# Optimization experiments

Hardware: AMD Instinct MI355X
Metric: run time of the kernel (lower is better)

## Reference

```python
import jax, jax.numpy as jnp
import numpy as np

INPUT_DIM = 256
EMBED_DIM = 256
NUM_HEADS = 8
HEAD_DIM = EMBED_DIM // NUM_HEADS
N_TOKENS = 11136
N_BATCH = 16


def _xavier(key, shape):
    fan_out, fan_in = shape
    bound = np.sqrt(6.0 / (fan_in + fan_out)).astype(np.float32)
    return jax.random.uniform(key, shape, jnp.float32, -bound, bound)


def setup_inputs() -> dict:
    key = jax.random.key(0)
    k_x, k_ids, k_qkv, k_o = jax.random.split(key, 4)
    x = jax.random.normal(k_x, (N_TOKENS, INPUT_DIM), jnp.float32)
    batch_ids = jnp.sort(jax.random.randint(k_ids, (N_TOKENS,), 0, N_BATCH)).astype(jnp.int32)
    qkv_w = _xavier(k_qkv, (3 * EMBED_DIM, INPUT_DIM))
    qkv_b = jnp.zeros((3 * EMBED_DIM,), jnp.float32)
    o_w = _xavier(k_o, (EMBED_DIM, EMBED_DIM))
    o_b = jnp.zeros((EMBED_DIM,), jnp.float32)
    return {"x": x, "batch_ids": batch_ids, "qkv_w": qkv_w, "qkv_b": qkv_b,
            "o_w": o_w, "o_b": o_b}


def reference(x, batch_ids, qkv_w, qkv_b, o_w, o_b):
    # batch_ids is concrete metadata (mirrors np.unique on CPU in the original).
    ids = np.asarray(batch_ids)
    vals, counts = np.unique(ids, return_counts=True)
    B = len(vals)
    S = int(counts.max())
    offsets = np.concatenate([np.zeros(1, np.int64), np.cumsum(counts)[:-1]])
    seg = np.searchsorted(vals, ids)               # segment index per token
    pos = np.arange(ids.shape[0]) - offsets[seg]   # position within segment

    qkv = x @ qkv_w.T + qkv_b                      # [N, 3E]
    # pad_sequence with padding_value=1 -> scatter tokens into an all-ones buffer
    fin = jnp.ones((B, S, 3 * EMBED_DIM), qkv.dtype).at[seg, pos].set(qkv)
    # padded rows sum to exactly 3E (all ones) -> mask True marks padding
    pad_mask = fin.sum(-1) >= fin.shape[-1]        # [B, S]

    qkv4 = fin.reshape(B, S, NUM_HEADS, 3 * HEAD_DIM).transpose(0, 2, 1, 3)
    q, k, v = jnp.split(qkv4, 3, axis=-1)          # each [B, H, S, hd]

    logits = jnp.einsum('bhqd,bhkd->bhqk', q, k) * (HEAD_DIM ** -0.5)
    logits = jnp.where(pad_mask[:, None, None, :], -jnp.inf, logits)
    attn = jax.nn.softmax(logits, axis=-1)         # [B, H, S, S]

    out = jnp.einsum('bhqk,bhkd->bhqd', attn, v)
    out = out.transpose(0, 2, 1, 3).reshape(B, S, EMBED_DIM)
    out = out[seg, pos]                            # unpad -> [N, E]
    return out @ o_w.T + o_b
```

## Files before the change

### kernel.cpp

```cpp
#include <hip/hip_runtime.h>
#include <stdint.h>


#define N_TOK 11136
#define E 256
#define H 8
#define HD 32

typedef __attribute__((ext_vector_type(8))) __bf16 bf16x8;
typedef __attribute__((ext_vector_type(8))) unsigned short u16x8;
typedef __attribute__((ext_vector_type(4))) float f32x4;

__device__ __forceinline__ unsigned short f2bf(float f) {
  unsigned int u = __float_as_uint(f);
  u = (u + 0x7FFFu + ((u >> 16) & 1u)) >> 16;
  return (unsigned short)u;
}
__device__ __forceinline__ float bf2f(unsigned short s) {
  return __uint_as_float(((unsigned int)s) << 16);
}
__device__ __forceinline__ bf16x8 ld8(const unsigned short* p) {
  return *(const bf16x8*)p;
}

__global__ void k_offsets(const int* __restrict__ ids, int* __restrict__ offs) {
  int b = threadIdx.x;
  if (b > 16) return;
  int lo = 0, hi = N_TOK;
  while (lo < hi) { int mid = (lo + hi) >> 1; if (ids[mid] < b) lo = mid + 1; else hi = mid; }
  offs[b] = lo;
}

#define QK_BSTRIDE 264
#define QSCALE (0.17677669529663687f * 1.4426950408889634f)
__global__ __launch_bounds__(256, 3) void k_qkv(
    const float* __restrict__ x, const float* __restrict__ qw,
    const float* __restrict__ qkv_b,
    unsigned short* __restrict__ Qb, unsigned short* __restrict__ Kb,
    unsigned short* __restrict__ Vt) {
  __shared__ __align__(16) unsigned short Bhi[48 * QK_BSTRIDE];
  __shared__ __align__(16) unsigned short Blo[48 * QK_BSTRIDE];
  int tid = threadIdx.x;
  int w = tid >> 6, lane = tid & 63, m = lane & 15, quad = lane >> 4;
  int col0 = blockIdx.y * 48;

  {
    const float4* qw4 = (const float4*)(qw + (size_t)col0 * E);
#pragma unroll
    for (int i = 0; i < 12; ++i) {
      int flat = i * 256 + tid;
      float4 v = qw4[flat];
      int row = flat >> 6, kq = flat & 63;
      ushort4 hv, lv;
      hv.x = f2bf(v.x); lv.x = f2bf(v.x - bf2f(hv.x));
      hv.y = f2bf(v.y); lv.y = f2bf(v.y - bf2f(hv.y));
      hv.z = f2bf(v.z); lv.z = f2bf(v.z - bf2f(hv.z));
      hv.w = f2bf(v.w); lv.w = f2bf(v.w - bf2f(hv.w));
      *(ushort4*)(Bhi + row * QK_BSTRIDE + kq * 4) = hv;
      *(ushort4*)(Blo + row * QK_BSTRIDE + kq * 4) = lv;
    }
  }
  __syncthreads();

  int base = blockIdx.x * 64 + w * 16;
  const float* ap = x + (size_t)(base + m) * E;
  f32x4 acc[3] = {};
  float4 c0 = *(const float4*)(ap + quad * 8);
  float4 c1 = *(const float4*)(ap + quad * 8 + 4);
  for (int kc = 0; kc < 8; ++kc) {
    float4 u0 = c0, u1 = c1;
    if (kc < 7) {
      c0 = *(const float4*)(ap + (kc + 1) * 32 + quad * 8);
      c1 = *(const float4*)(ap + (kc + 1) * 32 + quad * 8 + 4);
    }
    int ko = kc * 32 + quad * 8;
    float vv[8] = {u0.x, u0.y, u0.z, u0.w, u1.x, u1.y, u1.z, u1.w};
    u16x8 hr, lr_;
#pragma unroll
    for (int i = 0; i < 8; ++i) {
      unsigned short hh = f2bf(vv[i]);
      hr[i] = hh;
      lr_[i] = f2bf(vv[i] - bf2f(hh));
    }
    bf16x8 ah = __builtin_bit_cast(bf16x8, hr);
    bf16x8 al = __builtin_bit_cast(bf16x8, lr_);
#pragma unroll
    for (int t = 0; t < 3; ++t) {
      bf16x8 bh = ld8(Bhi + (16 * t + m) * QK_BSTRIDE + ko);
      bf16x8 bl = ld8(Blo + (16 * t + m) * QK_BSTRIDE + ko);
      acc[t] = __builtin_amdgcn_mfma_f32_16x16x32_bf16(ah, bh, acc[t], 0, 0, 0);
      acc[t] = __builtin_amdgcn_mfma_f32_16x16x32_bf16(ah, bl, acc[t], 0, 0, 0);
      acc[t] = __builtin_amdgcn_mfma_f32_16x16x32_bf16(al, bh, acc[t], 0, 0, 0);
    }
  }
#pragma unroll
  for (int t = 0; t < 3; ++t) {
    int j = col0 + 16 * t + m;
    int hd = j / 96;
    int rr = j - hd * 96;
    float bias = qkv_b[j];
    int tokb = base + quad * 4;
    if (rr < 64) {
      float qsc = (rr < 32) ? QSCALE : 1.0f;
      unsigned short* dst = (rr < 32) ? (Qb + (size_t)hd * N_TOK * HD + rr)
                                      : (Kb + (size_t)hd * N_TOK * HD + (rr - 32));
#pragma unroll
      for (int r = 0; r < 4; ++r)
        dst[(size_t)(tokb + r) * HD] = f2bf((acc[t][r] + bias) * qsc);
    } else {
      int d = rr - 64;
      ushort4 pk;
      pk.x = f2bf(acc[t][0] + bias); pk.y = f2bf(acc[t][1] + bias);
      pk.z = f2bf(acc[t][2] + bias); pk.w = f2bf(acc[t][3] + bias);
      *(ushort4*)(Vt + (size_t)(hd * HD + d) * N_TOK + tokb) = pk;
    }
  }
}

#define PSTRIDE 72
__global__ __launch_bounds__(256, 4) void k_attn(
    const int* __restrict__ ids, const int* __restrict__ offs,
    const unsigned short* __restrict__ Qb, const unsigned short* __restrict__ Kb,
    const unsigned short* __restrict__ Vt,
    unsigned short* __restrict__ attnb) {
  __shared__ __align__(16) unsigned short Kl[2][64 * 32];
  __shared__ __align__(16) unsigned short Vl[2][32 * 64];
  __shared__ __align__(16) unsigned short ldsP[4][16 * PSTRIDE];
  __shared__ int bred[8];
  int tid = threadIdx.x;
  int w = tid >> 6, lane = tid & 63;
  int m = lane & 15, quad = lane >> 4;
  int h = blockIdx.y;
  int tok0 = blockIdx.x * 64;
  int q0 = tok0 + w * 16;
  unsigned short* P = ldsP[w];
  int tok = q0 + m;
  int b = ids[tok];
  int st = offs[b], en = offs[b + 1];
  int kmin = st, kmax = en, stM = st, enm = en;
#pragma unroll
  for (int d = 1; d <= 8; d <<= 1) {
    kmin = min(kmin, __shfl_xor(kmin, d));
    kmax = max(kmax, __shfl_xor(kmax, d));
    stM  = max(stM,  __shfl_xor(stM,  d));
    enm  = min(enm,  __shfl_xor(enm,  d));
  }
  if (lane == 0) { bred[w] = kmin; bred[4 + w] = kmax; }
  __syncthreads();
  int kminB = min(min(bred[0], bred[1]), min(bred[2], bred[3]));
  int kmaxB = max(max(bred[4], bred[5]), max(bred[6], bred[7]));
  int k0beg = kminB & ~63;

  const unsigned short* Kbase = Qb ? Kb + (size_t)h * N_TOK * HD : Kb;
  const unsigned short* Vbase = Vt + (size_t)h * HD * N_TOK;
  bf16x8 qf = ld8(Qb + (size_t)(h * N_TOK + tok) * HD + quad * 8);

  int krow = w * 16 + (lane >> 2);
  int kgof = (lane & 3) * 8;
  int vrow = w * 8 + (lane >> 3);
  int vgof = (lane & 7) * 8;

  bf16x8 kg = ld8(Kbase + (size_t)(k0beg + krow) * HD + kgof);
  bf16x8 vg = ld8(Vbase + (size_t)vrow * N_TOK + k0beg + vgof);
  *(bf16x8*)(&Kl[0][krow * 32 + kgof]) = kg;
  *(bf16x8*)(&Vl[0][vrow * 64 + vgof]) = vg;
  __syncthreads();

  float lsum = 0.f;
  f32x4 o0 = {}, o1 = {};
  int buf = 0;
  for (int k0 = k0beg; k0 < kmaxB; k0 += 64) {
    int k1 = (k0 + 64 < kmaxB) ? (k0 + 64) : k0;
    kg = ld8(Kbase + (size_t)(k1 + krow) * HD + kgof);
    vg = ld8(Vbase + (size_t)vrow * N_TOK + k1 + vgof);
    const unsigned short* Kc = &Kl[buf][0];
    const unsigned short* Vc = &Vl[buf][0];
    f32x4 s[4];
#pragma unroll
    for (int i = 0; i < 4; ++i) {
      bf16x8 kf = ld8(Kc + (16 * i + m) * 32 + quad * 8);
      f32x4 z = {};
      s[i] = __builtin_amdgcn_mfma_f32_16x16x32_bf16(kf, qf, z, 0, 0, 0);
    }
    bool interior = (k0 >= stM && k0 + 64 <= enm);
    int jb = k0 + quad * 4;
#pragma unroll
    for (int i = 0; i < 4; ++i) {
      float p[4];
#pragma unroll
      for (int r = 0; r < 4; ++r) {
        float sv = s[i][r];
        if (!interior) {
          int j = jb + 16 * i + r;
          sv = (j >= st && j < en) ? sv : -3e38f;
        }
        float e;
        asm("v_exp_f32 %0, %1" : "=v"(e) : "v"(sv));
        p[r] = e;
      }
      lsum += (p[0] + p[1]) + (p[2] + p[3]);
      unsigned int b0 = __float_as_uint(p[0]) + 0x8000u;
      unsigned int b1 = __float_as_uint(p[1]) + 0x8000u;
      unsigned int b2 = __float_as_uint(p[2]) + 0x8000u;
      unsigned int b3 = __float_as_uint(p[3]) + 0x8000u;
      uint2 pk;
      pk.x = (b1 & 0xFFFF0000u) | (b0 >> 16);
      pk.y = (b3 & 0xFFFF0000u) | (b2 >> 16);
      *(uint2*)(P + m * PSTRIDE + 16 * i + quad * 4) = pk;
    }
#pragma unroll
    for (int c = 0; c < 2; ++c) {
      bf16x8 pf  = ld8(P + m * PSTRIDE + 32 * c + quad * 8);
      bf16x8 vf0 = ld8(Vc + m * 64 + 32 * c + quad * 8);
      bf16x8 vf1 = ld8(Vc + (16 + m) * 64 + 32 * c + quad * 8);
      o0 = __builtin_amdgcn_mfma_f32_16x16x32_bf16(vf0, pf, o0, 0, 0, 0);
      o1 = __builtin_amdgcn_mfma_f32_16x16x32_bf16(vf1, pf, o1, 0, 0, 0);
    }
    *(bf16x8*)(&Kl[buf ^ 1][krow * 32 + kgof]) = kg;
    *(bf16x8*)(&Vl[buf ^ 1][vrow * 64 + vgof]) = vg;
    __syncthreads();
    buf ^= 1;
  }
  lsum += __shfl_xor(lsum, 16);
  lsum += __shfl_xor(lsum, 32);
  float inv = 1.0f / lsum;
  ushort4 pk0, pk1;
  pk0.x = f2bf(o0[0] * inv); pk0.y = f2bf(o0[1] * inv);
  pk0.z = f2bf(o0[2] * inv); pk0.w = f2bf(o0[3] * inv);
  pk1.x = f2bf(o1[0] * inv); pk1.y = f2bf(o1[1] * inv);
  pk1.z = f2bf(o1[2] * inv); pk1.w = f2bf(o1[3] * inv);
  *(ushort4*)(attnb + (size_t)tok * E + h * HD + quad * 4) = pk0;
  *(ushort4*)(attnb + (size_t)tok * E + h * HD + 16 + quad * 4) = pk1;
}

__global__ __launch_bounds__(256, 2) void k_oproj(
    const unsigned short* __restrict__ attnb, const float* __restrict__ ow,
    const float* __restrict__ ob, float* __restrict__ out) {
  __shared__ __align__(16) unsigned short Bo[64 * QK_BSTRIDE];
  int tid = threadIdx.x;
  int w = tid >> 6, lane = tid & 63, m = lane & 15, quad = lane >> 4;
  int tok0 = blockIdx.x * 64, col0 = blockIdx.y * 64;
  {
    const float4* ow4 = (const float4*)(ow + (size_t)col0 * E);
#pragma unroll
    for (int i = 0; i < 16; ++i) {
      int flat = i * 256 + tid;
      float4 v = ow4[flat];
      int row = flat >> 6, kq = flat & 63;
      ushort4 hv;
      hv.x = f2bf(v.x); hv.y = f2bf(v.y); hv.z = f2bf(v.z); hv.w = f2bf(v.w);
      *(ushort4*)(Bo + row * QK_BSTRIDE + kq * 4) = hv;
    }
  }
  __syncthreads();
  f32x4 acc[4] = {};
  int arow = tok0 + 16 * w + m;
  for (int kc = 0; kc < 8; ++kc) {
    int ko = kc * 32 + quad * 8;
    bf16x8 a = ld8(attnb + (size_t)arow * E + ko);
#pragma unroll
    for (int t = 0; t < 4; ++t) {
      bf16x8 b = ld8(Bo + (16 * t + m) * QK_BSTRIDE + ko);
      acc[t] = __builtin_amdgcn_mfma_f32_16x16x32_bf16(a, b, acc[t], 0, 0, 0);
    }
  }
#pragma unroll
  for (int t = 0; t < 4; ++t) {
    int j = col0 + 16 * t + m;
    float bias = ob[j];
#pragma unroll
    for (int r = 0; r < 4; ++r) {
      int tok = tok0 + 16 * w + quad * 4 + r;
      out[(size_t)tok * E + j] = acc[t][r] + bias;
    }
  }
}

extern "C" void kernel_launch(void* const* d_in, const int* in_sizes, int n_in,
                              void* d_out, int out_size, void* d_ws, size_t ws_size,
                              hipStream_t stream) {
  const float* x   = (const float*)d_in[0];
  const int*   ids = (const int*)d_in[1];
  const float* qw  = (const float*)d_in[2];
  const float* qb  = (const float*)d_in[3];
  const float* ow  = (const float*)d_in[4];
  const float* ob  = (const float*)d_in[5];
  float* out = (float*)d_out;

  char* p = (char*)d_ws;
  auto alloc = [&](size_t bytes) {
    char* r = p;
    p += (bytes + 255) & ~(size_t)255;
    return r;
  };
  int* offs = (int*)alloc(32 * sizeof(int));
  unsigned short* Qb  = (unsigned short*)alloc((size_t)N_TOK * E * 2);
  unsigned short* Kb  = (unsigned short*)alloc((size_t)N_TOK * E * 2);
  unsigned short* Vt  = (unsigned short*)alloc((size_t)N_TOK * E * 2);
  unsigned short* att = (unsigned short*)alloc((size_t)N_TOK * E * 2);

  k_offsets<<<dim3(1), dim3(64), 0, stream>>>(ids, offs);
  k_qkv<<<dim3(N_TOK / 64, 16), dim3(256), 0, stream>>>(x, qw, qb, Qb, Kb, Vt);
  k_attn<<<dim3(N_TOK / 64, H), dim3(256), 0, stream>>>(ids, offs, Qb, Kb, Vt, att);
  k_oproj<<<dim3(N_TOK / 64, E / 64), dim3(256), 0, stream>>>(att, ow, ob, out);
}
```

Before: 163.2 us.

## Pre-split inputs and weights to bf16 hi/lo in a separate kernel

```diff
diff --git a/kernel.cpp b/kernel.cpp
--- a/kernel.cpp
+++ b/kernel.cpp
@@ -31,10 +31,49 @@
   offs[b] = lo;
 }
 
+__global__ void k_split(const float* __restrict__ x, const float* __restrict__ qw,
+                        const float* __restrict__ ow,
+                        unsigned short* __restrict__ xhi, unsigned short* __restrict__ xlo,
+                        unsigned short* __restrict__ whi, unsigned short* __restrict__ wlo,
+                        unsigned short* __restrict__ owb) {
+  const int NX4 = N_TOK * E / 4;
+  const int NW4 = 3 * E * E / 4;
+  const int NO4 = E * E / 4;
+  int total = NX4 + NW4 + NO4;
+  for (int i = blockIdx.x * blockDim.x + threadIdx.x; i < total;
+       i += gridDim.x * blockDim.x) {
+    if (i < NX4) {
+      float4 v = ((const float4*)x)[i];
+      ushort4 hv, lv;
+      hv.x = f2bf(v.x); lv.x = f2bf(v.x - bf2f(hv.x));
+      hv.y = f2bf(v.y); lv.y = f2bf(v.y - bf2f(hv.y));
+      hv.z = f2bf(v.z); lv.z = f2bf(v.z - bf2f(hv.z));
+      hv.w = f2bf(v.w); lv.w = f2bf(v.w - bf2f(hv.w));
+      ((ushort4*)xhi)[i] = hv; ((ushort4*)xlo)[i] = lv;
+    } else if (i < NX4 + NW4) {
+      int j = i - NX4;
+      float4 v = ((const float4*)qw)[j];
+      ushort4 hv, lv;
+      hv.x = f2bf(v.x); lv.x = f2bf(v.x - bf2f(hv.x));
+      hv.y = f2bf(v.y); lv.y = f2bf(v.y - bf2f(hv.y));
+      hv.z = f2bf(v.z); lv.z = f2bf(v.z - bf2f(hv.z));
+      hv.w = f2bf(v.w); lv.w = f2bf(v.w - bf2f(hv.w));
+      ((ushort4*)whi)[j] = hv; ((ushort4*)wlo)[j] = lv;
+    } else {
+      int j = i - NX4 - NW4;
+      float4 v = ((const float4*)ow)[j];
+      ushort4 hv;
+      hv.x = f2bf(v.x); hv.y = f2bf(v.y); hv.z = f2bf(v.z); hv.w = f2bf(v.w);
+      ((ushort4*)owb)[j] = hv;
+    }
+  }
+}
+
 #define QK_BSTRIDE 264
 #define QSCALE (0.17677669529663687f * 1.4426950408889634f)
 __global__ __launch_bounds__(256, 3) void k_qkv(
-    const float* __restrict__ x, const float* __restrict__ qw,
+    const unsigned short* __restrict__ xhi, const unsigned short* __restrict__ xlo,
+    const unsigned short* __restrict__ whi, const unsigned short* __restrict__ wlo,
     const float* __restrict__ qkv_b,
     unsigned short* __restrict__ Qb, unsigned short* __restrict__ Kb,
     unsigned short* __restrict__ Vt) {
@@ -42,55 +81,42 @@
   __shared__ __align__(16) unsigned short Blo[48 * QK_BSTRIDE];
   int tid = threadIdx.x;
   int w = tid >> 6, lane = tid & 63, m = lane & 15, quad = lane >> 4;
-  int col0 = blockIdx.y * 48;
+  int col0 = blockIdx.x * 48;
+  int base0 = blockIdx.y * 128;
 
   {
-    const float4* qw4 = (const float4*)(qw + (size_t)col0 * E);
-#pragma unroll
-    for (int i = 0; i < 12; ++i) {
+    const u16x8* wh8 = (const u16x8*)(whi + (size_t)col0 * E);
+    const u16x8* wl8 = (const u16x8*)(wlo + (size_t)col0 * E);
+#pragma unroll
+    for (int i = 0; i < 6; ++i) {
       int flat = i * 256 + tid;
-      float4 v = qw4[flat];
-      int row = flat >> 6, kq = flat & 63;
-      ushort4 hv, lv;
-      hv.x = f2bf(v.x); lv.x = f2bf(v.x - bf2f(hv.x));
-      hv.y = f2bf(v.y); lv.y = f2bf(v.y - bf2f(hv.y));
-      hv.z = f2bf(v.z); lv.z = f2bf(v.z - bf2f(hv.z));
-      hv.w = f2bf(v.w); lv.w = f2bf(v.w - bf2f(hv.w));
-      *(ushort4*)(Bhi + row * QK_BSTRIDE + kq * 4) = hv;
-      *(ushort4*)(Blo + row * QK_BSTRIDE + kq * 4) = lv;
+      int row = flat >> 5, c8 = flat & 31;
+      *(u16x8*)(Bhi + row * QK_BSTRIDE + c8 * 8) = wh8[flat];
+      *(u16x8*)(Blo + row * QK_BSTRIDE + c8 * 8) = wl8[flat];
     }
   }
   __syncthreads();
 
-  int base = blockIdx.x * 64 + w * 16;
-  const float* ap = x + (size_t)(base + m) * E;
-  f32x4 acc[3] = {};
-  float4 c0 = *(const float4*)(ap + quad * 8);
-  float4 c1 = *(const float4*)(ap + quad * 8 + 4);
+  f32x4 acc[2][3] = {};
   for (int kc = 0; kc < 8; ++kc) {
-    float4 u0 = c0, u1 = c1;
-    if (kc < 7) {
-      c0 = *(const float4*)(ap + (kc + 1) * 32 + quad * 8);
-      c1 = *(const float4*)(ap + (kc + 1) * 32 + quad * 8 + 4);
-    }
     int ko = kc * 32 + quad * 8;
-    float vv[8] = {u0.x, u0.y, u0.z, u0.w, u1.x, u1.y, u1.z, u1.w};
-    u16x8 hr, lr_;
-#pragma unroll
-    for (int i = 0; i < 8; ++i) {
-      unsigned short hh = f2bf(vv[i]);
-      hr[i] = hh;
-      lr_[i] = f2bf(vv[i] - bf2f(hh));
-    }
-    bf16x8 ah = __builtin_bit_cast(bf16x8, hr);
-    bf16x8 al = __builtin_bit_cast(bf16x8, lr_);
+    bf16x8 ah[2], al[2];
+#pragma unroll
+    for (int mt = 0; mt < 2; ++mt) {
+      int arow = base0 + mt * 64 + w * 16 + m;
+      ah[mt] = ld8(xhi + (size_t)arow * E + ko);
+      al[mt] = ld8(xlo + (size_t)arow * E + ko);
+    }
 #pragma unroll
     for (int t = 0; t < 3; ++t) {
       bf16x8 bh = ld8(Bhi + (16 * t + m) * QK_BSTRIDE + ko);
       bf16x8 bl = ld8(Blo + (16 * t + m) * QK_BSTRIDE + ko);
-      acc[t] = __builtin_amdgcn_mfma_f32_16x16x32_bf16(ah, bh, acc[t], 0, 0, 0);
-      acc[t] = __builtin_amdgcn_mfma_f32_16x16x32_bf16(ah, bl, acc[t], 0, 0, 0);
-      acc[t] = __builtin_amdgcn_mfma_f32_16x16x32_bf16(al, bh, acc[t], 0, 0, 0);
+#pragma unroll
+      for (int mt = 0; mt < 2; ++mt) {
+        acc[mt][t] = __builtin_amdgcn_mfma_f32_16x16x32_bf16(ah[mt], bh, acc[mt][t], 0, 0, 0);
+        acc[mt][t] = __builtin_amdgcn_mfma_f32_16x16x32_bf16(ah[mt], bl, acc[mt][t], 0, 0, 0);
+        acc[mt][t] = __builtin_amdgcn_mfma_f32_16x16x32_bf16(al[mt], bh, acc[mt][t], 0, 0, 0);
+      }
     }
   }
 #pragma unroll
@@ -99,20 +125,23 @@
     int hd = j / 96;
     int rr = j - hd * 96;
     float bias = qkv_b[j];
-    int tokb = base + quad * 4;
-    if (rr < 64) {
-      float qsc = (rr < 32) ? QSCALE : 1.0f;
-      unsigned short* dst = (rr < 32) ? (Qb + (size_t)hd * N_TOK * HD + rr)
-                                      : (Kb + (size_t)hd * N_TOK * HD + (rr - 32));
-#pragma unroll
-      for (int r = 0; r < 4; ++r)
-        dst[(size_t)(tokb + r) * HD] = f2bf((acc[t][r] + bias) * qsc);
-    } else {
-      int d = rr - 64;
-      ushort4 pk;
-      pk.x = f2bf(acc[t][0] + bias); pk.y = f2bf(acc[t][1] + bias);
-      pk.z = f2bf(acc[t][2] + bias); pk.w = f2bf(acc[t][3] + bias);
-      *(ushort4*)(Vt + (size_t)(hd * HD + d) * N_TOK + tokb) = pk;
+#pragma unroll
+    for (int mt = 0; mt < 2; ++mt) {
+      int tokb = base0 + mt * 64 + w * 16 + quad * 4;
+      if (rr < 64) {
+        float qsc = (rr < 32) ? QSCALE : 1.0f;
+        unsigned short* dst = (rr < 32) ? (Qb + (size_t)hd * N_TOK * HD + rr)
+                                        : (Kb + (size_t)hd * N_TOK * HD + (rr - 32));
+#pragma unroll
+        for (int r = 0; r < 4; ++r)
+          dst[(size_t)(tokb + r) * HD] = f2bf((acc[mt][t][r] + bias) * qsc);
+      } else {
+        int d = rr - 64;
+        ushort4 pk;
+        pk.x = f2bf(acc[mt][t][0] + bias); pk.y = f2bf(acc[mt][t][1] + bias);
+        pk.z = f2bf(acc[mt][t][2] + bias); pk.w = f2bf(acc[mt][t][3] + bias);
+        *(ushort4*)(Vt + (size_t)(hd * HD + d) * N_TOK + tokb) = pk;
+      }
     }
   }
 }
@@ -151,7 +180,7 @@
   int kmaxB = max(max(bred[4], bred[5]), max(bred[6], bred[7]));
   int k0beg = kminB & ~63;
 
-  const unsigned short* Kbase = Qb ? Kb + (size_t)h * N_TOK * HD : Kb;
+  const unsigned short* Kbase = Kb + (size_t)h * N_TOK * HD;
   const unsigned short* Vbase = Vt + (size_t)h * HD * N_TOK;
   bf16x8 qf = ld8(Qb + (size_t)(h * N_TOK + tok) * HD + quad * 8);
 
@@ -234,22 +263,19 @@
 }
 
 __global__ __launch_bounds__(256, 2) void k_oproj(
-    const unsigned short* __restrict__ attnb, const float* __restrict__ ow,
+    const unsigned short* __restrict__ attnb, const unsigned short* __restrict__ owb,
     const float* __restrict__ ob, float* __restrict__ out) {
   __shared__ __align__(16) unsigned short Bo[64 * QK_BSTRIDE];
   int tid = threadIdx.x;
   int w = tid >> 6, lane = tid & 63, m = lane & 15, quad = lane >> 4;
   int tok0 = blockIdx.x * 64, col0 = blockIdx.y * 64;
   {
-    const float4* ow4 = (const float4*)(ow + (size_t)col0 * E);
-#pragma unroll
-    for (int i = 0; i < 16; ++i) {
+    const u16x8* o8 = (const u16x8*)(owb + (size_t)col0 * E);
+#pragma unroll
+    for (int i = 0; i < 8; ++i) {
       int flat = i * 256 + tid;
-      float4 v = ow4[flat];
-      int row = flat >> 6, kq = flat & 63;
-      ushort4 hv;
-      hv.x = f2bf(v.x); hv.y = f2bf(v.y); hv.z = f2bf(v.z); hv.w = f2bf(v.w);
-      *(ushort4*)(Bo + row * QK_BSTRIDE + kq * 4) = hv;
+      int row = flat >> 5, c8 = flat & 31;
+      *(u16x8*)(Bo + row * QK_BSTRIDE + c8 * 8) = o8[flat];
     }
   }
   __syncthreads();
@@ -294,13 +320,19 @@
     return r;
   };
   int* offs = (int*)alloc(32 * sizeof(int));
+  unsigned short* xhi = (unsigned short*)alloc((size_t)N_TOK * E * 2);
+  unsigned short* xlo = (unsigned short*)alloc((size_t)N_TOK * E * 2);
+  unsigned short* whi = (unsigned short*)alloc((size_t)3 * E * E * 2);
+  unsigned short* wlo = (unsigned short*)alloc((size_t)3 * E * E * 2);
+  unsigned short* owb = (unsigned short*)alloc((size_t)E * E * 2);
   unsigned short* Qb  = (unsigned short*)alloc((size_t)N_TOK * E * 2);
   unsigned short* Kb  = (unsigned short*)alloc((size_t)N_TOK * E * 2);
   unsigned short* Vt  = (unsigned short*)alloc((size_t)N_TOK * E * 2);
   unsigned short* att = (unsigned short*)alloc((size_t)N_TOK * E * 2);
 
   k_offsets<<<dim3(1), dim3(64), 0, stream>>>(ids, offs);
-  k_qkv<<<dim3(N_TOK / 64, 16), dim3(256), 0, stream>>>(x, qw, qb, Qb, Kb, Vt);
+  k_split<<<dim3(1712), dim3(256), 0, stream>>>(x, qw, ow, xhi, xlo, whi, wlo, owb);
+  k_qkv<<<dim3(16, N_TOK / 128), dim3(256), 0, stream>>>(xhi, xlo, whi, wlo, qb, Qb, Kb, Vt);
   k_attn<<<dim3(N_TOK / 64, H), dim3(256), 0, stream>>>(ids, offs, Qb, Kb, Vt, att);
-  k_oproj<<<dim3(N_TOK / 64, E / 64), dim3(256), 0, stream>>>(att, ow, ob, out);
-}
+  k_oproj<<<dim3(N_TOK / 64, E / 64), dim3(256), 0, stream>>>(att, owb, ob, out);
+}
```

Measured after the change: 157.2 us. 1.04x faster.
